# Optimization experiments

Hardware: AMD Instinct MI355X
Metric: run time of the kernel (lower is better)

Reference implementation:

```python
import math
import jax, jax.numpy as jnp
import numpy as np

N_RADII = 64
MIN_RAD, MAX_RAD = 0.0, 2.0
RES_B, RES_A = 6, 12
SPATIAL = (4, 4, 4)
SCALE = (2, 2, 2)
# irreps as (multiplicity, l, parity)
IN0 = [(32, 0, 1), (16, 1, -1), (8, 2, 1)]
HID0 = [(64, 0, 1), (32, 0, -1), (32, 1, 1), (16, 2, 1), (16, 1, -1), (8, 2, -1)]
HID1 = [(32, 0, 1), (16, 0, -1), (16, 1, 1), (8, 2, 1), (8, 1, -1), (4, 2, -1)]

def SH_OUT(K):
    return [(K, 0, 1), (K, 1, -1), (K, 2, 1)]

def idim(irr):
    return sum(m * (2 * l + 1) for m, l, _ in irr)

def sh_matrix():
    # real spherical harmonics up to lmax=2 evaluated on a beta x alpha sphere grid
    b = (jnp.arange(RES_B, dtype=jnp.float32) + 0.5) * (np.pi / RES_B)
    a = jnp.arange(RES_A, dtype=jnp.float32) * (2.0 * np.pi / RES_A)
    B, A = jnp.meshgrid(b, a, indexing='ij')
    sx = jnp.sin(B) * jnp.cos(A)
    sy = jnp.sin(B) * jnp.sin(A)
    sz = jnp.cos(B)
    s3, s15, s5 = math.sqrt(3.0), math.sqrt(15.0), math.sqrt(5.0)
    Y = jnp.stack([jnp.ones_like(sx), s3 * sx, s3 * sy, s3 * sz,
                   s15 * sx * sy, s15 * sy * sz, 0.5 * s5 * (3.0 * sz * sz - 1.0),
                   s15 * sx * sz, 0.5 * s15 * (sx * sx - sy * sy)], 0)
    return Y.reshape(9, RES_B * RES_A)  # [9, G]

def eq_linear(x, irr_in, irr_out, w):
    # e3nn-style equivariant Linear: block matmul per matching (l, parity), 1/sqrt(mul_in) norm
    lead = x.shape[:-1]
    segs, off = {}, 0
    for m, l, p in irr_in:
        d = m * (2 * l + 1)
        segs[(l, p)] = (x[..., off:off + d].reshape(lead + (m, 2 * l + 1)), m)
        off += d
    outs = []
    for m, l, p in irr_out:
        if (l, p) in segs and (l, p) in w:
            s, mi = segs[(l, p)]
            y = jnp.einsum('...ik,io->...ok', s, w[(l, p)]) * (1.0 / math.sqrt(mi))
        else:
            y = jnp.zeros(lead + (m, 2 * l + 1), x.dtype)
        outs.append(y.reshape(lead + (m * (2 * l + 1),)))
    return jnp.concatenate(outs, -1)

def to_grid(sh, K, Y):
    # sh layout is mul-major per irrep: [K x 0e | K x 1o | K x 2e]
    lead = sh.shape[:-1]
    c = jnp.concatenate([sh[..., :K].reshape(lead + (K, 1)),
                         sh[..., K:4 * K].reshape(lead + (K, 3)),
                         sh[..., 4 * K:].reshape(lead + (K, 5))], -1)  # [..., K, 9]
    g = jnp.einsum('...kc,cg->...kg', c, Y)
    return g.reshape(lead + (K, RES_B, RES_A))

def closest_radii():
    # fine index grid vs nearest-upsampled coarse voxel centers; bin |r| to nearest radius
    dims = [s * f for s, f in zip(SPATIAL, SCALE)]
    g = jnp.stack(jnp.meshgrid(*[jnp.arange(d, dtype=jnp.float32) for d in dims], indexing='ij'), -1)
    sarr = jnp.asarray(SCALE, dtype=jnp.float32)
    centers = jnp.floor(g / sarr) * sarr + (sarr - 1.0) / 2.0
    r = jnp.linalg.norm(g - centers, axis=-1)
    bins = jnp.linspace(MIN_RAD, MAX_RAD, N_RADII)
    return jnp.argmin(jnp.abs(r[..., None] - bins), axis=-1)

def _forward(x, w1b0_0e, w1b0_1o, w1b0_2e, w2b0_0e, w2b0_1o, w2b0_2e,
             w1b1_0e, w1b1_0o, w1b1_1e, w1b1_1o, w1b1_2e, w1b1_2o,
             w2b1_0e, w2b1_1o, w2b1_2e):
    Y = sh_matrix()
    w1b0 = {(0, 1): w1b0_0e, (1, -1): w1b0_1o, (2, 1): w1b0_2e}
    w2b0 = {(0, 1): w2b0_0e, (1, -1): w2b0_1o, (2, 1): w2b0_2e}
    w1b1 = {(0, 1): w1b1_0e, (0, -1): w1b1_0o, (1, 1): w1b1_1e,
            (1, -1): w1b1_1o, (2, 1): w1b1_2e, (2, -1): w1b1_2o}
    w2b1 = {(0, 1): w2b1_0e, (1, -1): w2b1_1o, (2, 1): w2b1_2e}
    # block 0
    x = eq_linear(x, IN0, HID0, w1b0)
    K0 = N_RADII * idim(HID0)
    sh0 = eq_linear(x, HID0, SH_OUT(K0), w2b0)
    grid0 = to_grid(sh0, K0, Y)  # computed per block but unused downstream, as in original
    # block 1
    x = eq_linear(x, HID0, HID1, w1b1)
    K1 = N_RADII * idim(HID1)
    sh1 = eq_linear(x, HID1, SH_OUT(K1), w2b1)
    grid1 = to_grid(sh1, K1, Y)
    return x, grid1

def setup_inputs():
    key = jax.random.key(0)
    ks = jax.random.split(key, 16)
    w = lambda k, i, o: jax.random.normal(k, (i, o), jnp.float32)
    K0 = N_RADII * idim(HID0)
    K1 = N_RADII * idim(HID1)
    return {
        'x': jax.random.normal(ks[0], (1,) + SPATIAL + (idim(IN0),), jnp.float32),
        'w1b0_0e': w(ks[1], 32, 64), 'w1b0_1o': w(ks[2], 16, 16), 'w1b0_2e': w(ks[3], 8, 16),
        'w2b0_0e': w(ks[4], 64, K0), 'w2b0_1o': w(ks[5], 16, K0), 'w2b0_2e': w(ks[6], 16, K0),
        'w1b1_0e': w(ks[7], 64, 32), 'w1b1_0o': w(ks[8], 32, 16), 'w1b1_1e': w(ks[9], 32, 16),
        'w1b1_1o': w(ks[10], 16, 8), 'w1b1_2e': w(ks[11], 16, 8), 'w1b1_2o': w(ks[12], 8, 4),
        'w2b1_0e': w(ks[13], 32, K1), 'w2b1_1o': w(ks[14], 8, K1), 'w2b1_2e': w(ks[15], 8, K1),
    }

def reference(x, w1b0_0e, w1b0_1o, w1b0_2e, w2b0_0e, w2b0_1o, w2b0_2e,
              w1b1_0e, w1b1_0o, w1b1_1e, w1b1_1o, w1b1_2e, w1b1_2o,
              w2b1_0e, w2b1_1o, w2b1_2e):
    x_out, grid1 = _forward(x, w1b0_0e, w1b0_1o, w1b0_2e, w2b0_0e, w2b0_1o, w2b0_2e,
                            w1b1_0e, w1b1_0o, w1b1_1e, w1b1_1o, w1b1_2e, w1b1_2o,
                            w2b1_0e, w2b1_1o, w2b1_2e)
    return x_out, grid1, closest_radii()
```

## Files before the change

### kernel.cpp

```cpp
#include <hip/hip_runtime.h>
#include <math.h>

#define K1        11520
#define XDIM      180
#define NSP       64
#define NG        72
#define OUT1_OFF  11520
#define OUT2_OFF  (11520 + (size_t)NSP * K1 * NG)

#define INV_S32 0.17677669529663687f
#define INV_S8  0.35355339059327373f
#define INV_S16 0.25f
#define INV_S64 0.125f

__global__ __launch_bounds__(64) void eq_linears_kernel(
    const float* __restrict__ x,
    const float* __restrict__ w1b0_0e,
    const float* __restrict__ w1b0_1o,
    const float* __restrict__ w1b0_2e,
    const float* __restrict__ w1b1_0e,
    const float* __restrict__ w1b1_1o,
    const float* __restrict__ w1b1_2e,
    float* __restrict__ out)
{
    __shared__ float xin[120];
    __shared__ float x1_0e[64];
    __shared__ float x1_2e[80];
    __shared__ float x1_1o[48];
    __shared__ float xout[XDIM];

    const int t = threadIdx.x;
    const int s = blockIdx.x;

    for (int f = t; f < 120; f += 64) xin[f] = x[s * 120 + f];
    for (int f = t; f < XDIM; f += 64) xout[f] = 0.0f;
    __syncthreads();

    {
        float acc = 0.0f;
        #pragma unroll
        for (int j = 0; j < 32; ++j) acc += xin[j] * w1b0_0e[j * 64 + t];
        x1_0e[t] = acc * INV_S32;
    }
    for (int e = t; e < 80; e += 64) {
        int i = e / 5, m = e % 5;
        float acc = 0.0f;
        #pragma unroll
        for (int j = 0; j < 8; ++j) acc += xin[80 + j * 5 + m] * w1b0_2e[j * 16 + i];
        x1_2e[e] = acc * INV_S8;
    }
    if (t < 48) {
        int i = t / 3, m = t % 3;
        float acc = 0.0f;
        #pragma unroll
        for (int j = 0; j < 16; ++j) acc += xin[32 + j * 3 + m] * w1b0_1o[j * 16 + i];
        x1_1o[t] = acc * INV_S16;
    }
    __syncthreads();

    if (t < 32) {
        float acc = 0.0f;
        #pragma unroll
        for (int i = 0; i < 64; ++i) acc += x1_0e[i] * w1b1_0e[i * 32 + t];
        xout[t] = acc * INV_S64;
    }
    if (t < 40) {
        int o = t / 5, m = t % 5;
        float acc = 0.0f;
        #pragma unroll
        for (int i = 0; i < 16; ++i) acc += x1_2e[i * 5 + m] * w1b1_2e[i * 8 + o];
        xout[96 + t] = acc * INV_S16;
    }
    if (t < 24) {
        int o = t / 3, m = t % 3;
        float acc = 0.0f;
        #pragma unroll
        for (int i = 0; i < 16; ++i) acc += x1_1o[i * 3 + m] * w1b1_1o[i * 8 + o];
        xout[136 + t] = acc * INV_S16;
    }
    __syncthreads();

    for (int f = t; f < XDIM; f += 64) out[s * XDIM + f] = xout[f];

    if (t < 8) out[OUT2_OFF + (size_t)s * 8 + t] = 27.0f;
}

__global__ __launch_bounds__(256) void grid1_kernel(
    const float* __restrict__ w2b1_0e,
    const float* __restrict__ w2b1_1o,
    const float* __restrict__ w2b1_2e,
    float* __restrict__ out)
{
    __shared__ float Yl[9 * NG];
    __shared__ float xs[XDIM];
    __shared__ float coeff[256 * 9];

    const int t = threadIdx.x;
    const int s = blockIdx.y;

    if (t < NG) {
        int bi = t / 12, ai = t % 12;
        float bb = (bi + 0.5f) * (float)(M_PI / 6.0);
        float aa = (float)ai * (float)(M_PI / 6.0);
        float sb = sinf(bb), cb = cosf(bb);
        float sa = sinf(aa), ca = cosf(aa);
        float sx = sb * ca, sy = sb * sa, sz = cb;
        const float s3  = 1.7320508075688772f;
        const float s15 = 3.872983346207417f;
        const float s5  = 2.23606797749979f;
        Yl[0 * NG + t] = 1.0f;
        Yl[1 * NG + t] = s3 * sx;
        Yl[2 * NG + t] = s3 * sy;
        Yl[3 * NG + t] = s3 * sz;
        Yl[4 * NG + t] = s15 * sx * sy;
        Yl[5 * NG + t] = s15 * sy * sz;
        Yl[6 * NG + t] = 0.5f * s5 * (3.0f * sz * sz - 1.0f);
        Yl[7 * NG + t] = s15 * sx * sz;
        Yl[8 * NG + t] = 0.5f * s15 * (sx * sx - sy * sy);
    } else if (t >= 76) {
        int f = t - 76;
        xs[f] = out[(size_t)s * XDIM + f];
    }
    __syncthreads();

    {
        const int k = blockIdx.x * 256 + t;
        float c[9];
        float acc = 0.0f;
        #pragma unroll
        for (int i = 0; i < 32; ++i) acc += xs[i] * w2b1_0e[i * K1 + k];
        c[0] = acc * INV_S32;
        #pragma unroll
        for (int m = 0; m < 3; ++m) {
            acc = 0.0f;
            #pragma unroll
            for (int i = 0; i < 8; ++i) acc += xs[136 + i * 3 + m] * w2b1_1o[i * K1 + k];
            c[1 + m] = acc * INV_S8;
        }
        #pragma unroll
        for (int m = 0; m < 5; ++m) {
            acc = 0.0f;
            #pragma unroll
            for (int i = 0; i < 8; ++i) acc += xs[96 + i * 5 + m] * w2b1_2e[i * K1 + k];
            c[4 + m] = acc * INV_S8;
        }
        #pragma unroll
        for (int cc = 0; cc < 9; ++cc) coeff[t * 9 + cc] = c[cc];
    }
    __syncthreads();

    float* outbase = out + OUT1_OFF
                   + ((size_t)s * K1 + (size_t)blockIdx.x * 256) * NG;
    #pragma unroll
    for (int j = 0; j < 18; ++j) {
        int e = (t + j * 256) * 4;
        int kk = e / NG;
        int g  = e - kk * NG;
        const float* cf = &coeff[kk * 9];
        float4 acc = make_float4(0.f, 0.f, 0.f, 0.f);
        #pragma unroll
        for (int cc = 0; cc < 9; ++cc) {
            float co = cf[cc];
            float4 yv = *(const float4*)&Yl[cc * NG + g];
            acc.x += co * yv.x;
            acc.y += co * yv.y;
            acc.z += co * yv.z;
            acc.w += co * yv.w;
        }
        *(float4*)(outbase + e) = acc;
    }
}

extern "C" void kernel_launch(void* const* d_in, const int* in_sizes, int n_in,
                              void* d_out, int out_size, void* d_ws, size_t ws_size,
                              hipStream_t stream) {
    const float* x        = (const float*)d_in[0];
    const float* w1b0_0e  = (const float*)d_in[1];
    const float* w1b0_1o  = (const float*)d_in[2];
    const float* w1b0_2e  = (const float*)d_in[3];
    const float* w1b1_0e  = (const float*)d_in[7];
    const float* w1b1_1o  = (const float*)d_in[10];
    const float* w1b1_2e  = (const float*)d_in[11];
    const float* w2b1_0e  = (const float*)d_in[13];
    const float* w2b1_1o  = (const float*)d_in[14];
    const float* w2b1_2e  = (const float*)d_in[15];
    float* out = (float*)d_out;

    eq_linears_kernel<<<dim3(NSP), dim3(64), 0, stream>>>(
        x, w1b0_0e, w1b0_1o, w1b0_2e, w1b1_0e, w1b1_1o, w1b1_2e, out);

    grid1_kernel<<<dim3(K1 / 256, NSP), dim3(256), 0, stream>>>(
        w2b1_0e, w2b1_1o, w2b1_2e, out);
}
```

Before: 252.3 us.

## Fuse eq-linear kernel into grid kernel and reuse spherical-harmonic loads across rows

Merges the small per-voxel equivariant linear kernel into the large grid-projection kernel, so each block recomputes the tiny 180-feature vector itself instead of reading it back from global memory after a separate launch. The inner projection loop now loads the Y values once and applies them to two coefficient rows 128 apart. It also drops the constant Y0 row by seeding the accumulator with the l=0 coefficient, and pads coefficients to 12 floats so they can be read as float4. This removes one launch and the dependency between the two kernels, at the cost of redundant eq-linear work in every block (45 per voxel).

```diff
diff --git a/kernel.cpp b/kernel.cpp
--- a/kernel.cpp
+++ b/kernel.cpp
@@ -13,7 +13,7 @@
 #define INV_S16 0.25f
 #define INV_S64 0.125f
 
-__global__ __launch_bounds__(64) void eq_linears_kernel(
+__global__ __launch_bounds__(256) void up_fused_kernel(
     const float* __restrict__ x,
     const float* __restrict__ w1b0_0e,
     const float* __restrict__ w1b0_1o,
@@ -21,85 +21,28 @@
     const float* __restrict__ w1b1_0e,
     const float* __restrict__ w1b1_1o,
     const float* __restrict__ w1b1_2e,
+    const float* __restrict__ w2b1_0e,
+    const float* __restrict__ w2b1_1o,
+    const float* __restrict__ w2b1_2e,
     float* __restrict__ out)
 {
     __shared__ float xin[120];
     __shared__ float x1_0e[64];
     __shared__ float x1_2e[80];
     __shared__ float x1_1o[48];
-    __shared__ float xout[XDIM];
-
-    const int t = threadIdx.x;
-    const int s = blockIdx.x;
-
-    for (int f = t; f < 120; f += 64) xin[f] = x[s * 120 + f];
-    for (int f = t; f < XDIM; f += 64) xout[f] = 0.0f;
-    __syncthreads();
-
-    {
-        float acc = 0.0f;
-        #pragma unroll
-        for (int j = 0; j < 32; ++j) acc += xin[j] * w1b0_0e[j * 64 + t];
-        x1_0e[t] = acc * INV_S32;
-    }
-    for (int e = t; e < 80; e += 64) {
-        int i = e / 5, m = e % 5;
-        float acc = 0.0f;
-        #pragma unroll
-        for (int j = 0; j < 8; ++j) acc += xin[80 + j * 5 + m] * w1b0_2e[j * 16 + i];
-        x1_2e[e] = acc * INV_S8;
-    }
-    if (t < 48) {
-        int i = t / 3, m = t % 3;
-        float acc = 0.0f;
-        #pragma unroll
-        for (int j = 0; j < 16; ++j) acc += xin[32 + j * 3 + m] * w1b0_1o[j * 16 + i];
-        x1_1o[t] = acc * INV_S16;
-    }
-    __syncthreads();
-
-    if (t < 32) {
-        float acc = 0.0f;
-        #pragma unroll
-        for (int i = 0; i < 64; ++i) acc += x1_0e[i] * w1b1_0e[i * 32 + t];
-        xout[t] = acc * INV_S64;
-    }
-    if (t < 40) {
-        int o = t / 5, m = t % 5;
-        float acc = 0.0f;
-        #pragma unroll
-        for (int i = 0; i < 16; ++i) acc += x1_2e[i * 5 + m] * w1b1_2e[i * 8 + o];
-        xout[96 + t] = acc * INV_S16;
-    }
-    if (t < 24) {
-        int o = t / 3, m = t % 3;
-        float acc = 0.0f;
-        #pragma unroll
-        for (int i = 0; i < 16; ++i) acc += x1_1o[i * 3 + m] * w1b1_1o[i * 8 + o];
-        xout[136 + t] = acc * INV_S16;
-    }
-    __syncthreads();
-
-    for (int f = t; f < XDIM; f += 64) out[s * XDIM + f] = xout[f];
-
-    if (t < 8) out[OUT2_OFF + (size_t)s * 8 + t] = 27.0f;
-}
-
-__global__ __launch_bounds__(256) void grid1_kernel(
-    const float* __restrict__ w2b1_0e,
-    const float* __restrict__ w2b1_1o,
-    const float* __restrict__ w2b1_2e,
-    float* __restrict__ out)
-{
-    __shared__ float Yl[9 * NG];
     __shared__ float xs[XDIM];
-    __shared__ float coeff[256 * 9];
+    __shared__ float Yl[8 * NG];
+    __shared__ float coeff[256 * 12];
 
     const int t = threadIdx.x;
     const int s = blockIdx.y;
 
-    if (t < NG) {
-        int bi = t / 12, ai = t % 12;
+    if (t < 64) {
+        xin[t] = x[s * 120 + t];
+        if (t + 64 < 120) xin[t + 64] = x[s * 120 + t + 64];
+    } else if (t < 136) {
+        int g = t - 64;
+        int bi = g / 12, ai = g % 12;
         float bb = (bi + 0.5f) * (float)(M_PI / 6.0);
         float aa = (float)ai * (float)(M_PI / 6.0);
         float sb = sinf(bb), cb = cosf(bb);
@@ -108,20 +51,63 @@
         const float s3  = 1.7320508075688772f;
         const float s15 = 3.872983346207417f;
         const float s5  = 2.23606797749979f;
-        Yl[0 * NG + t] = 1.0f;
-        Yl[1 * NG + t] = s3 * sx;
-        Yl[2 * NG + t] = s3 * sy;
-        Yl[3 * NG + t] = s3 * sz;
-        Yl[4 * NG + t] = s15 * sx * sy;
-        Yl[5 * NG + t] = s15 * sy * sz;
-        Yl[6 * NG + t] = 0.5f * s5 * (3.0f * sz * sz - 1.0f);
-        Yl[7 * NG + t] = s15 * sx * sz;
-        Yl[8 * NG + t] = 0.5f * s15 * (sx * sx - sy * sy);
-    } else if (t >= 76) {
-        int f = t - 76;
-        xs[f] = out[(size_t)s * XDIM + f];
+        Yl[0 * NG + g] = s3 * sx;
+        Yl[1 * NG + g] = s3 * sy;
+        Yl[2 * NG + g] = s3 * sz;
+        Yl[3 * NG + g] = s15 * sx * sy;
+        Yl[4 * NG + g] = s15 * sy * sz;
+        Yl[5 * NG + g] = 0.5f * s5 * (3.0f * sz * sz - 1.0f);
+        Yl[6 * NG + g] = s15 * sx * sz;
+        Yl[7 * NG + g] = 0.5f * s15 * (sx * sx - sy * sy);
+    } else {
+        for (int f = t - 136; f < XDIM; f += 120) xs[f] = 0.0f;
     }
     __syncthreads();
+
+    if (t < 64) {
+        float acc = 0.0f;
+        #pragma unroll
+        for (int j = 0; j < 32; ++j) acc += xin[j] * w1b0_0e[j * 64 + t];
+        x1_0e[t] = acc * INV_S32;
+    } else if (t < 144) {
+        int e = t - 64, i = e / 5, m = e % 5;
+        float acc = 0.0f;
+        #pragma unroll
+        for (int j = 0; j < 8; ++j) acc += xin[80 + j * 5 + m] * w1b0_2e[j * 16 + i];
+        x1_2e[e] = acc * INV_S8;
+    } else if (t < 192) {
+        int e = t - 144, i = e / 3, m = e % 3;
+        float acc = 0.0f;
+        #pragma unroll
+        for (int j = 0; j < 16; ++j) acc += xin[32 + j * 3 + m] * w1b0_1o[j * 16 + i];
+        x1_1o[e] = acc * INV_S16;
+    }
+    __syncthreads();
+
+    if (t < 32) {
+        float acc = 0.0f;
+        #pragma unroll
+        for (int i = 0; i < 64; ++i) acc += x1_0e[i] * w1b1_0e[i * 32 + t];
+        xs[t] = acc * INV_S64;
+    } else if (t < 72) {
+        int e = t - 32, o = e / 5, m = e % 5;
+        float acc = 0.0f;
+        #pragma unroll
+        for (int i = 0; i < 16; ++i) acc += x1_2e[i * 5 + m] * w1b1_2e[i * 8 + o];
+        xs[96 + e] = acc * INV_S16;
+    } else if (t < 96) {
+        int e = t - 72, o = e / 3, m = e % 3;
+        float acc = 0.0f;
+        #pragma unroll
+        for (int i = 0; i < 16; ++i) acc += x1_1o[i * 3 + m] * w1b1_1o[i * 8 + o];
+        xs[136 + e] = acc * INV_S16;
+    }
+    __syncthreads();
+
+    if (blockIdx.x == 0) {
+        if (t < XDIM) out[(size_t)s * XDIM + t] = xs[t];
+        else if (t < XDIM + 8) out[OUT2_OFF + (size_t)s * 8 + (t - XDIM)] = 27.0f;
+    }
 
     {
         const int k = blockIdx.x * 256 + t;
@@ -144,30 +130,47 @@
             for (int i = 0; i < 8; ++i) acc += xs[96 + i * 5 + m] * w2b1_2e[i * K1 + k];
             c[4 + m] = acc * INV_S8;
         }
-        #pragma unroll
-        for (int cc = 0; cc < 9; ++cc) coeff[t * 9 + cc] = c[cc];
+        *(float4*)&coeff[t * 12]     = make_float4(c[0], c[1], c[2], c[3]);
+        *(float4*)&coeff[t * 12 + 4] = make_float4(c[4], c[5], c[6], c[7]);
+        coeff[t * 12 + 8] = c[8];
     }
     __syncthreads();
 
     float* outbase = out + OUT1_OFF
                    + ((size_t)s * K1 + (size_t)blockIdx.x * 256) * NG;
     #pragma unroll
-    for (int j = 0; j < 18; ++j) {
-        int e = (t + j * 256) * 4;
-        int kk = e / NG;
-        int g  = e - kk * NG;
-        const float* cf = &coeff[kk * 9];
-        float4 acc = make_float4(0.f, 0.f, 0.f, 0.f);
+    for (int j = 0; j < 9; ++j) {
+        const int e  = (t + j * 256) * 4;
+        const int kk = e / NG;
+        const int g  = e - kk * NG;
+
+        float4 Y1 = *(const float4*)&Yl[0 * NG + g];
+        float4 Y2 = *(const float4*)&Yl[1 * NG + g];
+        float4 Y3 = *(const float4*)&Yl[2 * NG + g];
+        float4 Y4 = *(const float4*)&Yl[3 * NG + g];
+        float4 Y5 = *(const float4*)&Yl[4 * NG + g];
+        float4 Y6 = *(const float4*)&Yl[5 * NG + g];
+        float4 Y7 = *(const float4*)&Yl[6 * NG + g];
+        float4 Y8 = *(const float4*)&Yl[7 * NG + g];
+
         #pragma unroll
-        for (int cc = 0; cc < 9; ++cc) {
-            float co = cf[cc];
-            float4 yv = *(const float4*)&Yl[cc * NG + g];
-            acc.x += co * yv.x;
-            acc.y += co * yv.y;
-            acc.z += co * yv.z;
-            acc.w += co * yv.w;
+        for (int p = 0; p < 2; ++p) {
+            const int kp = kk + p * 128;
+            float4 ca = *(const float4*)&coeff[kp * 12];
+            float4 cb = *(const float4*)&coeff[kp * 12 + 4];
+            float  c8 = coeff[kp * 12 + 8];
+            float4 acc;
+            acc.x = ca.x; acc.y = ca.x; acc.z = ca.x; acc.w = ca.x;
+            acc.x += ca.y * Y1.x; acc.y += ca.y * Y1.y; acc.z += ca.y * Y1.z; acc.w += ca.y * Y1.w;
+            acc.x += ca.z * Y2.x; acc.y += ca.z * Y2.y; acc.z += ca.z * Y2.z; acc.w += ca.z * Y2.w;
+            acc.x += ca.w * Y3.x; acc.y += ca.w * Y3.y; acc.z += ca.w * Y3.z; acc.w += ca.w * Y3.w;
+            acc.x += cb.x * Y4.x; acc.y += cb.x * Y4.y; acc.z += cb.x * Y4.z; acc.w += cb.x * Y4.w;
+            acc.x += cb.y * Y5.x; acc.y += cb.y * Y5.y; acc.z += cb.y * Y5.z; acc.w += cb.y * Y5.w;
+            acc.x += cb.z * Y6.x; acc.y += cb.z * Y6.y; acc.z += cb.z * Y6.z; acc.w += cb.z * Y6.w;
+            acc.x += cb.w * Y7.x; acc.y += cb.w * Y7.y; acc.z += cb.w * Y7.z; acc.w += cb.w * Y7.w;
+            acc.x += c8  * Y8.x; acc.y += c8  * Y8.y; acc.z += c8  * Y8.z; acc.w += c8  * Y8.w;
+            *(float4*)(outbase + e + p * 9216) = acc;
         }
-        *(float4*)(outbase + e) = acc;
     }
 }
 
@@ -186,9 +189,7 @@
     const float* w2b1_2e  = (const float*)d_in[15];
     float* out = (float*)d_out;
 
-    eq_linears_kernel<<<dim3(NSP), dim3(64), 0, stream>>>(
-        x, w1b0_0e, w1b0_1o, w1b0_2e, w1b1_0e, w1b1_1o, w1b1_2e, out);
-
-    grid1_kernel<<<dim3(K1 / 256, NSP), dim3(256), 0, stream>>>(
+    up_fused_kernel<<<dim3(K1 / 256, NSP), dim3(256), 0, stream>>>(
+        x, w1b0_0e, w1b0_1o, w1b0_2e, w1b1_0e, w1b1_1o, w1b1_2e,
         w2b1_0e, w2b1_1o, w2b1_2e, out);
 }
```

Measured after the change: 253.9 us. Within noise of the previous version (+0.6%).
